# Optimization experiments

Measured on AMD Instinct MI355X. Metric: run time of the kernel, lower is better.

## Reference

```python
import jax, jax.numpy as jnp
import numpy as np

B, T, D, H = 4, 2048, 512, 8
DH = D // H  # 64
EPS = 1e-5


def setup_inputs() -> dict:
    key = jax.random.key(0)
    ks = jax.random.split(key, 12)
    s = lambda k, shp, fan: jax.random.normal(k, shp, jnp.float32) * (fan ** -0.5)
    return {
        "x": jax.random.normal(ks[0], (B, T, D), jnp.float32),
        "ln1_g": jnp.ones((D,), jnp.float32),
        "ln1_b": jnp.zeros((D,), jnp.float32),
        "Wq": s(ks[1], (H, D, DH), D),  # per-head bias-free projections
        "Wk": s(ks[2], (H, D, DH), D),
        "Wv": s(ks[3], (H, D, DH), D),
        "Wproj": s(ks[4], (D, D), D),
        "bproj": jnp.zeros((D,), jnp.float32),
        "W1": s(ks[5], (D, 4 * D), D),
        "b1": jnp.zeros((4 * D,), jnp.float32),
        "W2": s(ks[6], (4 * D, D), 4 * D),
        "b2": jnp.zeros((D,), jnp.float32),
    }


def _layernorm(x, g, b):
    m = jnp.mean(x, axis=-1, keepdims=True)
    v = jnp.var(x, axis=-1, keepdims=True)
    return (x - m) * jax.lax.rsqrt(v + EPS) * g + b


def reference(x, ln1_g, ln1_b, Wq, Wk, Wv, Wproj, bproj, W1, b1, W2, b2):
    b, t, c = x.shape
    scale = c ** -0.5  # source scales by input channel dim, not head_size
    causal = jnp.tril(jnp.ones((t, t), bool))  # [T,T]

    # --- attention sublayer (pre-norm with ln1) ---
    h = _layernorm(x, ln1_g, ln1_b)
    q = jnp.einsum('btd,hde->bhte', h, Wq)
    k = jnp.einsum('btd,hde->bhte', h, Wk)
    v = jnp.einsum('btd,hde->bhte', h, Wv)
    scores = jnp.einsum('bhte,bhse->bhts', q, k) * scale  # [B,H,T,T]
    scores = jnp.where(causal, scores, -jnp.inf)
    att = jax.nn.softmax(scores, axis=-1)  # dropout = identity at inference
    o = jnp.einsum('bhts,bhse->bthe', att, v).reshape(b, t, c)  # concat heads
    sa = o @ Wproj + bproj
    x = x + sa

    # --- FFN sublayer (source reuses ln1, faithful) ---
    h2 = _layernorm(x, ln1_g, ln1_b)
    ff = jax.nn.relu(h2 @ W1 + b1) @ W2 + b2
    return x + ff
```

## Files before the change

kernel.cpp:

```cpp
#include <hip/hip_runtime.h>
#include <math.h>

#define B_ 4
#define T_ 2048
#define D_ 512
#define H_ 8
#define DH_ 64
#define BT_ 8192
#define FF_ 2048
#define EPS_ 1e-5f
#define SCALE_ 0.04419417382415922f
#define SC2_ 0.06375861151f
#define NEGINF_ -1e30f

typedef short b16x8 __attribute__((ext_vector_type(8)));
typedef short b16x4 __attribute__((ext_vector_type(4)));
typedef float f32x4 __attribute__((ext_vector_type(4)));

#define MFMA16(a, b, c) __builtin_amdgcn_mfma_f32_16x16x32_bf16(a, b, c, 0, 0, 0)
#define MFMA16K16(a, b, c) __builtin_amdgcn_mfma_f32_16x16x16bf16_1k(a, b, c, 0, 0, 0)

#define GLL16(gp, lp) \
    __builtin_amdgcn_global_load_lds((const __attribute__((address_space(1))) void*)(gp), \
                                     (__attribute__((address_space(3))) void*)(lp), 16, 0, 0)

#if __has_builtin(__builtin_amdgcn_exp2f)
#define EXP2F(x) __builtin_amdgcn_exp2f(x)
#else
#define EXP2F(x) exp2f(x)
#endif

static __device__ inline short f2bf(float f) {
    unsigned int u = __builtin_bit_cast(unsigned int, f);
    unsigned int r = (u + 0x7fffu + ((u >> 16) & 1u)) >> 16;
    return (short)r;
}
static __device__ inline short f2bf_trunc(float f) {
    return (short)(__builtin_bit_cast(unsigned int, f) >> 16);
}
static __device__ inline float bf2f(short s) {
    return __builtin_bit_cast(float, ((unsigned int)(unsigned short)s) << 16);
}

__global__ __launch_bounds__(256) void ln_kernel(const float* __restrict__ X,
        const float* __restrict__ G, const float* __restrict__ Bb,
        short* __restrict__ Y)
{
    int wave = threadIdx.x >> 6, t = threadIdx.x & 63;
    int row = blockIdx.x * 4 + wave;
    const float* xr = X + (size_t)row * D_;
    float4 v0 = *(const float4*)(xr + t * 4);
    float4 v1 = *(const float4*)(xr + 256 + t * 4);
    float sum = v0.x + v0.y + v0.z + v0.w + v1.x + v1.y + v1.z + v1.w;
    float ssq = v0.x*v0.x + v0.y*v0.y + v0.z*v0.z + v0.w*v0.w
              + v1.x*v1.x + v1.y*v1.y + v1.z*v1.z + v1.w*v1.w;
    #pragma unroll
    for (int off = 32; off > 0; off >>= 1) {
        sum += __shfl_down(sum, off);
        ssq += __shfl_down(ssq, off);
    }
    sum = __shfl(sum, 0);
    ssq = __shfl(ssq, 0);
    float mean = sum * (1.0f / D_);
    float var  = ssq * (1.0f / D_) - mean * mean;
    float rstd = rsqrtf(var + EPS_);

    float4 g0 = *(const float4*)(G + t * 4);
    float4 g1 = *(const float4*)(G + 256 + t * 4);
    float4 b0 = *(const float4*)(Bb + t * 4);
    float4 b1 = *(const float4*)(Bb + 256 + t * 4);
    short4 o0, o1;
    o0.x = f2bf((v0.x - mean) * rstd * g0.x + b0.x);
    o0.y = f2bf((v0.y - mean) * rstd * g0.y + b0.y);
    o0.z = f2bf((v0.z - mean) * rstd * g0.z + b0.z);
    o0.w = f2bf((v0.w - mean) * rstd * g0.w + b0.w);
    o1.x = f2bf((v1.x - mean) * rstd * g1.x + b1.x);
    o1.y = f2bf((v1.y - mean) * rstd * g1.y + b1.y);
    o1.z = f2bf((v1.z - mean) * rstd * g1.z + b1.z);
    o1.w = f2bf((v1.w - mean) * rstd * g1.w + b1.w);
    short* yr = Y + (size_t)row * D_;
    *(short4*)(yr + t * 4)       = o0;
    *(short4*)(yr + 256 + t * 4) = o1;
}

__global__ __launch_bounds__(256) void prep_kernel(
        const float* __restrict__ Wq, const float* __restrict__ Wk,
        const float* __restrict__ Wv, const float* __restrict__ Wp,
        const float* __restrict__ W1, const float* __restrict__ W2,
        short* __restrict__ wqkv, short* __restrict__ wpt,
        short* __restrict__ w1t, short* __restrict__ w2t)
{
    __shared__ float tile[32][33];
    int idx = blockIdx.x;
    const float* src; short* dst; int R, C, tx0, ty0;
    if (idx < 768) {
        int w = idx >> 8, rem = idx & 255;
        int hh = rem >> 5, t = rem & 31;
        const float* base = (w == 0) ? Wq : ((w == 1) ? Wk : Wv);
        src = base + hh * (D_ * DH_);
        dst = wqkv + w * (512 * 512) + hh * (DH_ * D_);
        R = 512; C = 64; tx0 = (t & 1) * 32; ty0 = (t >> 1) * 32;
    } else if (idx < 1024) {
        int t = idx - 768;
        src = Wp; dst = wpt; R = 512; C = 512;
        tx0 = (t & 15) * 32; ty0 = (t >> 4) * 32;
    } else if (idx < 2048) {
        int t = idx - 1024;
        src = W1; dst = w1t; R = 512; C = 2048;
        tx0 = (t & 63) * 32; ty0 = (t >> 6) * 32;
    } else {
        int t = idx - 2048;
        src = W2; dst = w2t; R = 2048; C = 512;
        tx0 = (t & 15) * 32; ty0 = (t >> 4) * 32;
    }
    int tx = threadIdx.x, ty = threadIdx.y;
    #pragma unroll
    for (int i = 0; i < 32; i += 8)
        tile[ty + i][tx] = src[(size_t)(ty0 + ty + i) * C + tx0 + tx];
    __syncthreads();
    #pragma unroll
    for (int i = 0; i < 32; i += 8)
        dst[(size_t)(tx0 + ty + i) * R + ty0 + tx] = f2bf(tile[tx][ty + i]);
}

__global__ __launch_bounds__(256) void mm64_kernel(const short* __restrict__ A,
        const short* __restrict__ Bt, void* __restrict__ C,
        const float* __restrict__ bias, const float* __restrict__ resid,
        int M, int N, int K, int relu, int out_bf16)
{
    __shared__ short As[2][128 * 32];
    __shared__ short Bs[2][64 * 32];
    const int tid = threadIdx.x;
    const int wave = tid >> 6, lane = tid & 63;
    const int quad = lane >> 4, l15 = lane & 15;
    const int m0 = blockIdx.x * 128, n0 = blockIdx.y * 64;
    const int mw = (wave & 1) * 64, nw = (wave >> 1) * 32;

#define STAGE_M64(bufi, kk) \
    { \
        for (int r = 0; r < 2; ++r) { \
            int c = r * 256 + tid; \
            int row = c >> 2, seg = (c & 3) ^ ((row >> 1) & 3); \
            GLL16(A + (size_t)(m0 + row) * K + (kk) + seg * 8, \
                  As[bufi] + (size_t)(r * 256 + wave * 64) * 8); \
        } \
        { \
            int row = tid >> 2, seg = (tid & 3) ^ ((row >> 1) & 3); \
            GLL16(Bt + (size_t)(n0 + row) * K + (kk) + seg * 8, \
                  Bs[bufi] + (size_t)(wave * 64) * 8); \
        } \
    }

    f32x4 acc[4][2];
    #pragma unroll
    for (int i = 0; i < 4; ++i)
        #pragma unroll
        for (int j = 0; j < 2; ++j)
            acc[i][j] = (f32x4){0.f, 0.f, 0.f, 0.f};

    STAGE_M64(0, 0);
    int buf = 0;
    for (int k0 = 0; k0 < K; k0 += 32) {
        __syncthreads();
        if (k0 + 32 < K) STAGE_M64(buf ^ 1, k0 + 32);
        b16x8 af[4], bf[2];
        #pragma unroll
        for (int i = 0; i < 4; ++i) {
            int row = mw + i * 16 + l15;
            af[i] = *(const b16x8*)(As[buf] + row * 32 + ((quad ^ ((row >> 1) & 3)) * 8));
        }
        #pragma unroll
        for (int j = 0; j < 2; ++j) {
            int row = nw + j * 16 + l15;
            bf[j] = *(const b16x8*)(Bs[buf] + row * 32 + ((quad ^ ((row >> 1) & 3)) * 8));
        }
        #pragma unroll
        for (int i = 0; i < 4; ++i)
            #pragma unroll
            for (int j = 0; j < 2; ++j)
                acc[i][j] = MFMA16(af[i], bf[j], acc[i][j]);
        buf ^= 1;
    }
#undef STAGE_M64

    #pragma unroll
    for (int i = 0; i < 4; ++i) {
        #pragma unroll
        for (int r = 0; r < 4; ++r) {
            size_t row = (size_t)(m0 + mw + i * 16 + quad * 4 + r);
            #pragma unroll
            for (int j = 0; j < 2; ++j) {
                int col = n0 + nw + j * 16 + l15;
                float v = acc[i][j][r];
                if (bias)  v += bias[col];
                if (resid) v += resid[row * N + col];
                if (relu)  v = fmaxf(v, 0.0f);
                if (out_bf16) ((short*)C)[row * N + col] = f2bf(v);
                else          ((float*)C)[row * N + col] = v;
            }
        }
    }
}

__global__ __launch_bounds__(256) void mm6464_kernel(const short* __restrict__ A,
        const short* __restrict__ Bt, void* __restrict__ C,
        const float* __restrict__ bias, const float* __restrict__ resid,
        int M, int N, int K, int relu, int out_bf16)
{
    __shared__ short As[2][64 * 32];
    __shared__ short Bs[2][64 * 32];
    const int tid = threadIdx.x;
    const int wave = tid >> 6, lane = tid & 63;
    const int quad = lane >> 4, l15 = lane & 15;
    const int m0 = blockIdx.x * 64, n0 = blockIdx.y * 64;
    const int nw = wave * 16;
    const int kcount = K / gridDim.z;
    const int kstart = blockIdx.z * kcount;
    const size_t cofs = (size_t)blockIdx.z * M * N;

#define STAGE_M66(bufi, kk) \
    { \
        int row = tid >> 2, seg = (tid & 3) ^ ((row >> 1) & 3); \
        GLL16(A + (size_t)(m0 + row) * K + (kk) + seg * 8, \
              As[bufi] + (size_t)(wave * 64) * 8); \
        GLL16(Bt + (size_t)(n0 + row) * K + (kk) + seg * 8, \
              Bs[bufi] + (size_t)(wave * 64) * 8); \
    }

    f32x4 acc[4];
    #pragma unroll
    for (int i = 0; i < 4; ++i) acc[i] = (f32x4){0.f, 0.f, 0.f, 0.f};

    STAGE_M66(0, kstart);
    int buf = 0;
    for (int k0 = kstart; k0 < kstart + kcount; k0 += 32) {
        __syncthreads();
        if (k0 + 32 < kstart + kcount) STAGE_M66(buf ^ 1, k0 + 32);
        b16x8 af[4], bf;
        #pragma unroll
        for (int i = 0; i < 4; ++i) {
            int row = i * 16 + l15;
            af[i] = *(const b16x8*)(As[buf] + row * 32 + ((quad ^ ((row >> 1) & 3)) * 8));
        }
        {
            int row = nw + l15;
            bf = *(const b16x8*)(Bs[buf] + row * 32 + ((quad ^ ((row >> 1) & 3)) * 8));
        }
        #pragma unroll
        for (int i = 0; i < 4; ++i)
            acc[i] = MFMA16(af[i], bf, acc[i]);
        buf ^= 1;
    }
#undef STAGE_M66

    #pragma unroll
    for (int i = 0; i < 4; ++i) {
        #pragma unroll
        for (int r = 0; r < 4; ++r) {
            size_t row = (size_t)(m0 + i * 16 + quad * 4 + r);
            int col = n0 + nw + l15;
            float v = acc[i][r];
            if (bias)  v += bias[col];
            if (resid) v += resid[row * N + col];
            if (relu)  v = fmaxf(v, 0.0f);
            if (out_bf16) ((short*)C)[cofs + row * N + col] = f2bf(v);
            else          ((float*)C)[cofs + row * N + col] = v;
        }
    }
}

__global__ __launch_bounds__(256) void ffn2_combine_kernel(
        const short* __restrict__ P, const float* __restrict__ x1,
        const float* __restrict__ b2, float* __restrict__ out)
{
    size_t idx = ((size_t)blockIdx.x * 256 + threadIdx.x) * 8;
    int col = (int)(idx & 511);
    b16x8 p0 = *(const b16x8*)(P + idx);
    b16x8 p1 = *(const b16x8*)(P + (size_t)BT_ * D_ + idx);
    float4 xa = *(const float4*)(x1 + idx);
    float4 xb = *(const float4*)(x1 + idx + 4);
    float4 ba = *(const float4*)(b2 + col);
    float4 bb = *(const float4*)(b2 + col + 4);
    float4 oa, ob;
    oa.x = xa.x + ba.x + bf2f(p0[0]) + bf2f(p1[0]);
    oa.y = xa.y + ba.y + bf2f(p0[1]) + bf2f(p1[1]);
    oa.z = xa.z + ba.z + bf2f(p0[2]) + bf2f(p1[2]);
    oa.w = xa.w + ba.w + bf2f(p0[3]) + bf2f(p1[3]);
    ob.x = xb.x + bb.x + bf2f(p0[4]) + bf2f(p1[4]);
    ob.y = xb.y + bb.y + bf2f(p0[5]) + bf2f(p1[5]);
    ob.z = xb.z + bb.z + bf2f(p0[6]) + bf2f(p1[6]);
    ob.w = xb.w + bb.w + bf2f(p0[7]) + bf2f(p1[7]);
    *(float4*)(out + idx)     = oa;
    *(float4*)(out + idx + 4) = ob;
}

__global__ __launch_bounds__(256) void attn_kernel(const short* __restrict__ qkv,
        short* __restrict__ Opart, float* __restrict__ Ml)
{
    __shared__ short Qs[64 * 72];
    __shared__ short Ks[64 * 64];
    __shared__ short Vt[64 * 64];

    const int tid = threadIdx.x;
    const int wave = tid >> 6, lane = tid & 63;
    const int quad = lane >> 4, l15 = lane & 15;
    const int bh = blockIdx.x;
    const int qi = 31 - (int)blockIdx.y;
    const int split = blockIdx.z;
    const int b = bh >> 3, h = bh & 7;
    const size_t tok0 = (size_t)b * T_;
    const int qrow_rel = wave * 16 + l15;
    const int half = (qi + 1) >> 1;
    const int klo = split ? half : 0;
    const int khi = split ? qi + 1 : half;
    const int pidx = split * 1024 + bh * 32 + qi;
    short* Op = Opart + (size_t)pidx * 4096;
    float* mlp = Ml + (size_t)pidx * 64;

    if (klo >= khi) {
        for (int i = tid; i < 2048; i += 256) ((int*)Op)[i] = 0;
        if (tid < 64) mlp[tid] = 0.0f;
        return;
    }

    #pragma unroll
    for (int r = 0; r < 2; ++r) {
        int c = r * 256 + tid;
        int tk = c >> 3;
        int seg = (c & 7) ^ (tk & 7);
        GLL16(qkv + (tok0 + qi * 64 + tk) * 1536 + h * 64 + seg * 8,
              Qs + (size_t)(r * 256 + wave * 64) * 8);
    }

    float lrow = 0.0f;
    f32x4 ot[4];
    #pragma unroll
    for (int dt = 0; dt < 4; ++dt) ot[dt] = (f32x4){0.f, 0.f, 0.f, 0.f};

    b16x8 qf[2];

    for (int kj = klo; kj < khi; ++kj) {
        __syncthreads();
        #pragma unroll
        for (int r = 0; r < 2; ++r) {
            int c = r * 256 + tid;
            int tk = c >> 3;
            int seg = (c & 7) ^ (tk & 7);
            GLL16(qkv + (tok0 + kj * 64 + tk) * 1536 + 512 + h * 64 + seg * 8,
                  Ks + (size_t)(r * 256 + wave * 64) * 8);
        }
        {
            int s = tid >> 5, tp = tid & 31;
            const short* g0 = qkv + (tok0 + kj * 64 + tp * 2) * 1536 + 1024 + h * 64 + s * 8;
            b16x8 v0 = *(const b16x8*)g0;
            b16x8 v1 = *(const b16x8*)(g0 + 1536);
            int* vo = (int*)Vt;
            int gg = tp >> 1, hlf = tp & 1;
            #pragma unroll
            for (int e = 0; e < 8; ++e) {
                int row = s * 8 + e;
                unsigned int pk = (unsigned int)(unsigned short)v0[e]
                                | ((unsigned int)(unsigned short)v1[e] << 16);
                vo[row * 32 + ((gg ^ (row & 15)) << 1) + hlf] = pk;
            }
        }
        __syncthreads();

        if (kj == klo) {
            #pragma unroll
            for (int kb = 0; kb < 2; ++kb) {
                int row = wave * 16 + l15;
                qf[kb] = *(const b16x8*)(Qs + row * 64 + (((kb * 4 + quad) ^ (row & 7)) * 8));
            }
        }

        f32x4 st[4];
        #pragma unroll
        for (int mt = 0; mt < 4; ++mt) st[mt] = (f32x4){0.f, 0.f, 0.f, 0.f};
        #pragma unroll
        for (int mt = 0; mt < 4; ++mt) {
            int trow = mt * 16 + l15;
            #pragma unroll
            for (int kb = 0; kb < 2; ++kb) {
                b16x8 kf = *(const b16x8*)(Ks + trow * 64 + (((kb * 4 + quad) ^ (trow & 7)) * 8));
                st[mt] = MFMA16(kf, qf[kb], st[mt]);
            }
        }

        const bool diag = (kj == qi);
        float rs = 0.0f;
        b16x4 pf[4];
        #pragma unroll
        for (int mt = 0; mt < 4; ++mt)
            #pragma unroll
            for (int r = 0; r < 4; ++r) {
                float s = st[mt][r];
                if (diag && (mt * 16 + quad * 4 + r) > qrow_rel) s = NEGINF_;
                float e = EXP2F(s * SC2_);
                rs += e;
                pf[mt][r] = f2bf_trunc(e);
            }
        rs += __shfl_xor(rs, 16);
        rs += __shfl_xor(rs, 32);
        lrow += rs;
        #pragma unroll
        for (int dt = 0; dt < 4; ++dt) {
            const short* vrow = Vt + (dt * 16 + l15) * 64;
            #pragma unroll
            for (int kt = 0; kt < 4; ++kt) {
                b16x4 vf = *(const b16x4*)(vrow + (((kt * 4 + quad) ^ l15) << 2));
                ot[dt] = MFMA16K16(vf, pf[kt], ot[dt]);
            }
        }
    }

    __syncthreads();
    float inv = 1.0f / lrow;
    #pragma unroll
    for (int dt = 0; dt < 4; ++dt) {
        b16x4 o4;
        o4[0] = f2bf(ot[dt][0] * inv);
        o4[1] = f2bf(ot[dt][1] * inv);
        o4[2] = f2bf(ot[dt][2] * inv);
        o4[3] = f2bf(ot[dt][3] * inv);
        *(b16x4*)(Qs + (size_t)qrow_rel * 72 + dt * 16 + quad * 4) = o4;
    }
    {
        int row = tid >> 2, ch = tid & 3;
        b16x8 lo = *(const b16x8*)(Qs + (size_t)row * 72 + ch * 16);
        b16x8 hi = *(const b16x8*)(Qs + (size_t)row * 72 + ch * 16 + 8);
        short* dst = Op + row * 64 + ch * 16;
        *(b16x8*)dst = lo;
        *(b16x8*)(dst + 8) = hi;
    }
    if (quad == 0) mlp[qrow_rel] = lrow;
}

__global__ __launch_bounds__(256) void attn_combine_kernel(
        const short* __restrict__ Opart, const float* __restrict__ Ml,
        short* __restrict__ Ob)
{
    int pair = blockIdx.x;
    int bh = pair >> 5, qi = pair & 31;
    int b = bh >> 3, h = bh & 7;
    int tid = threadIdx.x;
    const short* O1 = Opart + (size_t)pair * 4096;
    const short* O2 = Opart + (size_t)(1024 + pair) * 4096;
    const float* ml1 = Ml + (size_t)pair * 64;
    const float* ml2 = Ml + (size_t)(1024 + pair) * 64;
    int ch = tid & 7;
    #pragma unroll
    for (int it = 0; it < 2; ++it) {
        int row = it * 32 + (tid >> 3);
        float l1 = ml1[row], l2 = ml2[row];
        float inv = 1.0f / (l1 + l2);
        float w1 = l1 * inv, w2 = l2 * inv;
        b16x8 a = *(const b16x8*)(O1 + row * 64 + ch * 8);
        b16x8 c = *(const b16x8*)(O2 + row * 64 + ch * 8);
        b16x8 o;
        #pragma unroll
        for (int e = 0; e < 8; ++e)
            o[e] = f2bf(w1 * bf2f(a[e]) + w2 * bf2f(c[e]));
        short* dst = Ob + ((size_t)(b * T_ + qi * 64 + row)) * 512 + h * 64 + ch * 8;
        *(b16x8*)dst = o;
    }
}

extern "C" void kernel_launch(void* const* d_in, const int* in_sizes, int n_in,
                              void* d_out, int out_size, void* d_ws, size_t ws_size,
                              hipStream_t stream) {
    (void)in_sizes; (void)n_in; (void)out_size; (void)ws_size;
    const float* x     = (const float*)d_in[0];
    const float* ln_g  = (const float*)d_in[1];
    const float* ln_b  = (const float*)d_in[2];
    const float* Wq    = (const float*)d_in[3];
    const float* Wk    = (const float*)d_in[4];
    const float* Wv    = (const float*)d_in[5];
    const float* Wproj = (const float*)d_in[6];
    const float* bproj = (const float*)d_in[7];
    const float* W1    = (const float*)d_in[8];
    const float* b1    = (const float*)d_in[9];
    const float* W2    = (const float*)d_in[10];
    const float* b2    = (const float*)d_in[11];
    float* out = (float*)d_out;

    char* W = (char*)d_ws;
    short* hbuf  = (short*)(W + 0);
    short* qkvb  = (short*)(W + ((size_t)8  << 20));
    short* attno = (short*)(W + ((size_t)32 << 20));
    float* x1    = (float*)(W + ((size_t)40 << 20));
    short* ff1   = (short*)(W + ((size_t)56 << 20));
    short* wqkv  = (short*)(W + ((size_t)88 << 20));
    short* wpt   = (short*)(W + ((size_t)90 << 20));
    short* w1t   = (short*)(W + ((size_t)91 << 20));
    short* w2t   = (short*)(W + ((size_t)93 << 20));
    short* Opart = (short*)(W + ((size_t)56 << 20));
    float* Ml    = (float*)(W + ((size_t)72 << 20));
    short* Pffn  = (short*)(W + ((size_t)8  << 20));

    prep_kernel<<<dim3(3072), dim3(32, 8), 0, stream>>>(
        Wq, Wk, Wv, Wproj, W1, W2, wqkv, wpt, w1t, w2t);
    ln_kernel<<<dim3(BT_ / 4), dim3(256), 0, stream>>>(x, ln_g, ln_b, hbuf);
    mm64_kernel<<<dim3(64, 24), dim3(256), 0, stream>>>(hbuf, wqkv, qkvb,
        nullptr, nullptr, BT_, 1536, D_, 0, 1);
    attn_kernel<<<dim3(32, 32, 2), dim3(256), 0, stream>>>(qkvb, Opart, Ml);
    attn_combine_kernel<<<dim3(1024), dim3(256), 0, stream>>>(Opart, Ml, attno);
    mm6464_kernel<<<dim3(128, 8, 1), dim3(256), 0, stream>>>(attno, wpt, x1,
        bproj, x, BT_, D_, D_, 0, 0);
    ln_kernel<<<dim3(BT_ / 4), dim3(256), 0, stream>>>(x1, ln_g, ln_b, hbuf);
    mm64_kernel<<<dim3(64, 32), dim3(256), 0, stream>>>(hbuf, w1t, ff1,
        b1, nullptr, BT_, FF_, D_, 1, 1);
    mm6464_kernel<<<dim3(128, 8, 2), dim3(256), 0, stream>>>(ff1, w2t, Pffn,
        nullptr, nullptr, BT_, D_, FF_, 0, 1);
    ffn2_combine_kernel<<<dim3(2048), dim3(256), 0, stream>>>(Pffn, x1, b2, out);
}
```

Before: 274.2 us.

## Drop split-K for FFN2, widen mm6464 K-tile to 64, fuse epilogue

The 64x64 GEMM kernel now stages 64-wide K tiles with an 8-way XOR swizzle, which halves the number of loop iterations and barriers per K. The FFN2 GEMM no longer uses a two-way split-K with bf16 partials and a separate combine kernel. It writes fp32 output directly with the bias and residual fused into the epilogue, which removes one launch and the partial-buffer round trip. In exchange FFN2 runs with half as many blocks (1024), which lowers parallelism on the long K=2048 reduction. The attention scratch buffers are also moved to new workspace offsets.

```diff
diff --git a/kernel.cpp b/kernel.cpp
--- a/kernel.cpp
+++ b/kernel.cpp
@@ -207,48 +207,53 @@
         const float* __restrict__ bias, const float* __restrict__ resid,
         int M, int N, int K, int relu, int out_bf16)
 {
-    __shared__ short As[2][64 * 32];
-    __shared__ short Bs[2][64 * 32];
+    __shared__ short As[2][64 * 64];
+    __shared__ short Bs[2][64 * 64];
     const int tid = threadIdx.x;
     const int wave = tid >> 6, lane = tid & 63;
     const int quad = lane >> 4, l15 = lane & 15;
     const int m0 = blockIdx.x * 64, n0 = blockIdx.y * 64;
     const int nw = wave * 16;
-    const int kcount = K / gridDim.z;
-    const int kstart = blockIdx.z * kcount;
-    const size_t cofs = (size_t)blockIdx.z * M * N;
 
 #define STAGE_M66(bufi, kk) \
     { \
-        int row = tid >> 2, seg = (tid & 3) ^ ((row >> 1) & 3); \
-        GLL16(A + (size_t)(m0 + row) * K + (kk) + seg * 8, \
-              As[bufi] + (size_t)(wave * 64) * 8); \
-        GLL16(Bt + (size_t)(n0 + row) * K + (kk) + seg * 8, \
-              Bs[bufi] + (size_t)(wave * 64) * 8); \
+        for (int r = 0; r < 2; ++r) { \
+            int c = r * 256 + tid; \
+            int row = c >> 3, seg = (c & 7) ^ (row & 7); \
+            GLL16(A + (size_t)(m0 + row) * K + (kk) + seg * 8, \
+                  As[bufi] + (size_t)(r * 256 + wave * 64) * 8); \
+            GLL16(Bt + (size_t)(n0 + row) * K + (kk) + seg * 8, \
+                  Bs[bufi] + (size_t)(r * 256 + wave * 64) * 8); \
+        } \
     }
 
     f32x4 acc[4];
     #pragma unroll
     for (int i = 0; i < 4; ++i) acc[i] = (f32x4){0.f, 0.f, 0.f, 0.f};
 
-    STAGE_M66(0, kstart);
+    STAGE_M66(0, 0);
     int buf = 0;
-    for (int k0 = kstart; k0 < kstart + kcount; k0 += 32) {
+    for (int k0 = 0; k0 < K; k0 += 64) {
         __syncthreads();
-        if (k0 + 32 < kstart + kcount) STAGE_M66(buf ^ 1, k0 + 32);
-        b16x8 af[4], bf;
-        #pragma unroll
-        for (int i = 0; i < 4; ++i) {
-            int row = i * 16 + l15;
-            af[i] = *(const b16x8*)(As[buf] + row * 32 + ((quad ^ ((row >> 1) & 3)) * 8));
-        }
-        {
+        if (k0 + 64 < K) STAGE_M66(buf ^ 1, k0 + 64);
+        b16x8 af[4][2], bf[2];
+        #pragma unroll
+        for (int i = 0; i < 4; ++i)
+            #pragma unroll
+            for (int kb = 0; kb < 2; ++kb) {
+                int row = i * 16 + l15;
+                af[i][kb] = *(const b16x8*)(As[buf] + row * 64 + (((kb * 4 + quad) ^ (row & 7)) * 8));
+            }
+        #pragma unroll
+        for (int kb = 0; kb < 2; ++kb) {
             int row = nw + l15;
-            bf = *(const b16x8*)(Bs[buf] + row * 32 + ((quad ^ ((row >> 1) & 3)) * 8));
-        }
-        #pragma unroll
-        for (int i = 0; i < 4; ++i)
-            acc[i] = MFMA16(af[i], bf, acc[i]);
+            bf[kb] = *(const b16x8*)(Bs[buf] + row * 64 + (((kb * 4 + quad) ^ (row & 7)) * 8));
+        }
+        #pragma unroll
+        for (int kb = 0; kb < 2; ++kb)
+            #pragma unroll
+            for (int i = 0; i < 4; ++i)
+                acc[i] = MFMA16(af[i][kb], bf[kb], acc[i]);
         buf ^= 1;
     }
 #undef STAGE_M66
@@ -263,35 +268,10 @@
             if (bias)  v += bias[col];
             if (resid) v += resid[row * N + col];
             if (relu)  v = fmaxf(v, 0.0f);
-            if (out_bf16) ((short*)C)[cofs + row * N + col] = f2bf(v);
-            else          ((float*)C)[cofs + row * N + col] = v;
-        }
-    }
-}
-
-__global__ __launch_bounds__(256) void ffn2_combine_kernel(
-        const short* __restrict__ P, const float* __restrict__ x1,
-        const float* __restrict__ b2, float* __restrict__ out)
-{
-    size_t idx = ((size_t)blockIdx.x * 256 + threadIdx.x) * 8;
-    int col = (int)(idx & 511);
-    b16x8 p0 = *(const b16x8*)(P + idx);
-    b16x8 p1 = *(const b16x8*)(P + (size_t)BT_ * D_ + idx);
-    float4 xa = *(const float4*)(x1 + idx);
-    float4 xb = *(const float4*)(x1 + idx + 4);
-    float4 ba = *(const float4*)(b2 + col);
-    float4 bb = *(const float4*)(b2 + col + 4);
-    float4 oa, ob;
-    oa.x = xa.x + ba.x + bf2f(p0[0]) + bf2f(p1[0]);
-    oa.y = xa.y + ba.y + bf2f(p0[1]) + bf2f(p1[1]);
-    oa.z = xa.z + ba.z + bf2f(p0[2]) + bf2f(p1[2]);
-    oa.w = xa.w + ba.w + bf2f(p0[3]) + bf2f(p1[3]);
-    ob.x = xb.x + bb.x + bf2f(p0[4]) + bf2f(p1[4]);
-    ob.y = xb.y + bb.y + bf2f(p0[5]) + bf2f(p1[5]);
-    ob.z = xb.z + bb.z + bf2f(p0[6]) + bf2f(p1[6]);
-    ob.w = xb.w + bb.w + bf2f(p0[7]) + bf2f(p1[7]);
-    *(float4*)(out + idx)     = oa;
-    *(float4*)(out + idx + 4) = ob;
+            if (out_bf16) ((short*)C)[row * N + col] = f2bf(v);
+            else          ((float*)C)[row * N + col] = v;
+        }
+    }
 }
 
 __global__ __launch_bounds__(256) void attn_kernel(const short* __restrict__ qkv,
@@ -494,9 +474,8 @@
     short* wpt   = (short*)(W + ((size_t)90 << 20));
     short* w1t   = (short*)(W + ((size_t)91 << 20));
     short* w2t   = (short*)(W + ((size_t)93 << 20));
-    short* Opart = (short*)(W + ((size_t)56 << 20));
-    float* Ml    = (float*)(W + ((size_t)72 << 20));
-    short* Pffn  = (short*)(W + ((size_t)8  << 20));
+    short* Opart = (short*)(W + ((size_t)96 << 20));
+    float* Ml    = (float*)(W + ((size_t)112 << 20));
 
     prep_kernel<<<dim3(3072), dim3(32, 8), 0, stream>>>(
         Wq, Wk, Wv, Wproj, W1, W2, wqkv, wpt, w1t, w2t);
@@ -505,12 +484,11 @@
         nullptr, nullptr, BT_, 1536, D_, 0, 1);
     attn_kernel<<<dim3(32, 32, 2), dim3(256), 0, stream>>>(qkvb, Opart, Ml);
     attn_combine_kernel<<<dim3(1024), dim3(256), 0, stream>>>(Opart, Ml, attno);
-    mm6464_kernel<<<dim3(128, 8, 1), dim3(256), 0, stream>>>(attno, wpt, x1,
+    mm6464_kernel<<<dim3(128, 8), dim3(256), 0, stream>>>(attno, wpt, x1,
         bproj, x, BT_, D_, D_, 0, 0);
     ln_kernel<<<dim3(BT_ / 4), dim3(256), 0, stream>>>(x1, ln_g, ln_b, hbuf);
     mm64_kernel<<<dim3(64, 32), dim3(256), 0, stream>>>(hbuf, w1t, ff1,
         b1, nullptr, BT_, FF_, D_, 1, 1);
-    mm6464_kernel<<<dim3(128, 8, 2), dim3(256), 0, stream>>>(ff1, w2t, Pffn,
-        nullptr, nullptr, BT_, D_, FF_, 0, 1);
-    ffn2_combine_kernel<<<dim3(2048), dim3(256), 0, stream>>>(Pffn, x1, b2, out);
-}
+    mm6464_kernel<<<dim3(128, 8), dim3(256), 0, stream>>>(ff1, w2t, out,
+        b2, x1, BT_, D_, FF_, 0, 0);
+}
```

After: 257.1 us, median of 2. 6.2% less time.
